# Optimization experiments

Measured on AMD Instinct MI355X. Metric: run time of the kernel, lower is better.

The kernel has to match this reference:

```python
import jax, jax.numpy as jnp
import numpy as np

D = 1024; H = 8; HD = D // H; N_RHS = 4; B = 2; SQ = 1024; SKV = 512
VOCAB = 32000; NL = 6; FF = 4 * D
EPS = 1e-6


def rms(x, w):
    return x * jax.lax.rsqrt(jnp.mean(x * x, axis=-1, keepdims=True) + EPS) * w


def rotate_half(x):
    x1, x2 = jnp.split(x, 2, axis=-1)
    return jnp.concatenate([-x2, x1], axis=-1)


def rope_cos_sin(S):
    inv = 1.0 / (10000.0 ** (jnp.arange(0, HD, 2, dtype=jnp.float32) / HD))
    f = jnp.outer(jnp.arange(S, dtype=jnp.float32), inv)
    f = jnp.concatenate([f, f], axis=-1)  # [S, HD]
    return jnp.cos(f), jnp.sin(f)


def split_heads(t):
    b, s, _ = t.shape
    return t.reshape(b, s, H, HD).swapaxes(1, 2)  # [B,H,S,HD]


def mha_cross(x, kv, in_w, in_b, out_w, out_b):
    # torch nn.MultiheadAttention, batch_first, averaged attn weights
    q = split_heads(x @ in_w[:D].T + in_b[:D])
    k = split_heads(kv @ in_w[D:2 * D].T + in_b[D:2 * D])
    v = split_heads(kv @ in_w[2 * D:].T + in_b[2 * D:])
    a = jax.nn.softmax(jnp.einsum('bhqd,bhkd->bhqk', q, k) / jnp.sqrt(jnp.float32(HD)), axis=-1)
    o = jnp.einsum('bhqk,bhkd->bhqd', a, v).swapaxes(1, 2).reshape(x.shape)
    return o @ out_w.T + out_b, a.mean(axis=1)


def self_attn(x, wq, wk, wv, wo, cos, sin):
    q = split_heads(x @ wq.T)
    k = split_heads(x @ wk.T)
    v = split_heads(x @ wv.T)
    q = q * cos + rotate_half(q) * sin
    k = k * cos + rotate_half(k) * sin
    a = jax.nn.softmax(jnp.einsum('bhqd,bhkd->bhqk', q, k) / jnp.sqrt(jnp.float32(HD)), axis=-1)
    o = jnp.einsum('bhqk,bhkd->bhqd', a, v).swapaxes(1, 2).reshape(x.shape)
    return o @ wo.T


def forward(rh_hiddens, rh_confidences, query_hidden,
            ca_in_w, ca_in_b, ca_out_w, ca_out_b, cross_norm_w,
            ag_w1, ag_b1, ag_w2, ag_b2, ag_norm_w,
            gen_n1, gen_wq, gen_wk, gen_wv, gen_wo, gen_n2, gen_wg, gen_wu, gen_wd,
            gen_norm_w, lm_head_w, m_w1, m_b1, m_w2, m_b2):
    b = query_hidden.shape[0]
    # confidence-weighted KV: rh_hiddens [N,B,S,D], rh_confidences [B,N]
    weighted = rh_hiddens * rh_confidences.T[:, :, None, None]
    all_kv = weighted.transpose(1, 0, 2, 3).reshape(b, N_RHS * SKV, D)

    x = query_hidden
    attn_weights = None
    for i in range(2):
        residual = x
        x = rms(x, cross_norm_w[i])
        x, attn_weights = mha_cross(x, all_kv, ca_in_w[i], ca_in_b[i], ca_out_w[i], ca_out_b[i])
        x = x + residual

    # agreement signal from unweighted per-response summaries
    summaries = rh_hiddens.mean(axis=2).transpose(1, 0, 2).reshape(b, N_RHS * D)
    h = jax.nn.gelu(summaries @ ag_w1.T + ag_b1, approximate=False)
    agreement = rms(h @ ag_w2.T + ag_b2, ag_norm_w)
    x = x + agreement[:, None, :]

    cos, sin = rope_cos_sin(x.shape[1])  # broadcast over [B,H,S,HD]
    for l in range(NL):
        h = rms(x, gen_n1[l])
        x = x + self_attn(h, gen_wq[l], gen_wk[l], gen_wv[l], gen_wo[l], cos, sin)
        h = rms(x, gen_n2[l])
        ff = (jax.nn.silu(h @ gen_wg[l].T) * (h @ gen_wu[l].T)) @ gen_wd[l].T
        x = x + ff

    x = rms(x, gen_norm_w)
    logits = x @ lm_head_w.T
    pooled = x.mean(axis=1)
    meta = jax.nn.gelu(pooled @ m_w1.T + m_b1, approximate=False) @ m_w2.T + m_b2
    return logits, meta, attn_weights


def setup_inputs() -> dict:
    key = jax.random.key(0)
    ks = iter(jax.random.split(key, 40))
    s = 0.02
    rn = lambda *shape: jax.random.normal(next(ks), shape, dtype=jnp.float32) * s
    inp = {
        'rh_hiddens': jax.random.normal(next(ks), (N_RHS, B, SKV, D), dtype=jnp.float32),
        'rh_confidences': jax.random.uniform(next(ks), (B, N_RHS), dtype=jnp.float32),
        'rh_roles': jax.random.randint(next(ks), (B, N_RHS), 0, 8),
        'query_hidden': jax.random.normal(next(ks), (B, SQ, D), dtype=jnp.float32),
        'ca_in_w': rn(2, 3 * D, D), 'ca_in_b': rn(2, 3 * D),
        'ca_out_w': rn(2, D, D), 'ca_out_b': rn(2, D),
        'cross_norm_w': jnp.ones((2, D), jnp.float32),
        'ag_w1': rn(2 * D, N_RHS * D), 'ag_b1': rn(2 * D),
        'ag_w2': rn(D, 2 * D), 'ag_b2': rn(D),
        'ag_norm_w': jnp.ones((D,), jnp.float32),
        'gen_n1': jnp.ones((NL, D), jnp.float32),
        'gen_wq': rn(NL, D, D), 'gen_wk': rn(NL, D, D),
        'gen_wv': rn(NL, D, D), 'gen_wo': rn(NL, D, D),
        'gen_n2': jnp.ones((NL, D), jnp.float32),
        'gen_wg': rn(NL, FF, D), 'gen_wu': rn(NL, FF, D), 'gen_wd': rn(NL, D, FF),
        'gen_norm_w': jnp.ones((D,), jnp.float32),
        'lm_head_w': rn(VOCAB, D),
        'm_w1': rn(D // 4, D), 'm_b1': rn(D // 4),
        'm_w2': rn(3, D // 4), 'm_b2': rn(3),
    }
    return inp


def reference(rh_hiddens, rh_confidences, rh_roles, query_hidden,
              ca_in_w, ca_in_b, ca_out_w, ca_out_b, cross_norm_w,
              ag_w1, ag_b1, ag_w2, ag_b2, ag_norm_w,
              gen_n1, gen_wq, gen_wk, gen_wv, gen_wo, gen_n2, gen_wg, gen_wu, gen_wd,
              gen_norm_w, lm_head_w, m_w1, m_b1, m_w2, m_b2):
    # rh_roles is accepted but unused, matching the torch forward
    return forward(rh_hiddens, rh_confidences, query_hidden,
                   ca_in_w, ca_in_b, ca_out_w, ca_out_b, cross_norm_w,
                   ag_w1, ag_b1, ag_w2, ag_b2, ag_norm_w,
                   gen_n1, gen_wq, gen_wk, gen_wv, gen_wo, gen_n2, gen_wg, gen_wu, gen_wd,
                   gen_norm_w, lm_head_w, m_w1, m_b1, m_w2, m_b2)
```

## Files before the change

### kernel.cpp

```cpp
#include <hip/hip_runtime.h>
#include <math.h>

#define D_     1024
#define H_     8
#define HD_    128
#define NR_    4
#define B_     2
#define SQ_    1024
#define SKV_   512
#define SKVT_  2048
#define VOCAB_ 32000
#define NL_    6
#define FF_    4096
#define EPS_   1e-6f

typedef unsigned short u16;
typedef __attribute__((ext_vector_type(8))) __bf16 bf16x8;
typedef __attribute__((ext_vector_type(4))) float f32x4;

__device__ __forceinline__ u16 f2bf_rn(float f) {
    unsigned u = __float_as_uint(f);
    unsigned r = (u + 0x7FFFu + ((u >> 16) & 1u)) >> 16;
    return (u16)r;
}
__device__ __forceinline__ float bf2f(u16 h) {
    return __uint_as_float(((unsigned)h) << 16);
}
__device__ __forceinline__ void splitf(float v, u16& h, u16& l) {
    h = f2bf_rn(v);
    l = f2bf_rn(v - bf2f(h));
}

__device__ __forceinline__ void glds16(const u16* g, const u16* l) {
    __builtin_amdgcn_global_load_lds(
        (const __attribute__((address_space(1))) void*)g,
        (__attribute__((address_space(3))) void*)l,
        16, 0, 0);
}

enum { CM_F32 = 0, CM_PAIR = 1, CM_PAIRT = 2 };

template<int CMODE>
__global__ __launch_bounds__(256, 2)
void k_gemm_bf(const u16* __restrict__ Ah, const u16* __restrict__ Al,
               int lda, long long sAb, long long sAh,
               const u16* __restrict__ Bh, const u16* __restrict__ Bl,
               int ldb, long long sBb, long long sBh,
               float* __restrict__ Cf, u16* __restrict__ Ch, u16* __restrict__ Cl,
               int ldc, long long sCb, long long sCh,
               int K, int ZH, float scale, const float* __restrict__ bias)
{
    __shared__ u16 lds[16384];

    const int z  = blockIdx.z;
    const int zb = z / ZH, zh = z - zb * ZH;
    const long long offA = zb * sAb + zh * sAh;
    const long long offB = zb * sBb + zh * sBh;
    const long long offC = zb * sCb + zh * sCh;

    const int m0 = blockIdx.y << 7, n0 = blockIdx.x << 7;
    const int tid = threadIdx.x, lane = tid & 63, w = tid >> 6;
    const int wr = w >> 1, wc = w & 1;

    const u16* pAh = Ah + offA; const u16* pAl = Al + offA;
    const u16* pBh = Bh + offB; const u16* pBl = Bl + offB;

    f32x4 acc[4][4];
#pragma unroll
    for (int i = 0; i < 4; ++i)
#pragma unroll
        for (int j = 0; j < 4; ++j) acc[i][j] = (f32x4){0.f, 0.f, 0.f, 0.f};

    const int ks = lane >> 4, lr16 = lane & 15;

    for (int k0 = 0; k0 < K; k0 += 32) {
#pragma unroll
        for (int c = 0; c < 2; ++c) {
            const int chunk = w * 2 + c;
            const int slab = chunk >> 1, hf = chunk & 1;
            const int row = hf * 64 + lane;
            const int lbase = (slab * 128 + hf * 64) * 8;
            const long long ga = (long long)(m0 + row) * lda + (k0 + slab * 8);
            const long long gb = (long long)(n0 + row) * ldb + (k0 + slab * 8);
            glds16(pAh + ga, &lds[lbase]);
            glds16(pAl + ga, &lds[4096 + lbase]);
            glds16(pBh + gb, &lds[8192 + lbase]);
            glds16(pBl + gb, &lds[12288 + lbase]);
        }
        __syncthreads();

        bf16x8 bh[4], bl[4];
#pragma unroll
        for (int nj = 0; nj < 4; ++nj) {
            const int off = (ks * 128 + wc * 64 + nj * 16 + lr16) * 8;
            bh[nj] = *(const bf16x8*)&lds[8192 + off];
            bl[nj] = *(const bf16x8*)&lds[12288 + off];
        }
#pragma unroll
        for (int mi = 0; mi < 4; ++mi) {
            const int off = (ks * 128 + wr * 64 + mi * 16 + lr16) * 8;
            bf16x8 ah = *(const bf16x8*)&lds[off];
            bf16x8 al = *(const bf16x8*)&lds[4096 + off];
#pragma unroll
            for (int nj = 0; nj < 4; ++nj) {
                acc[mi][nj] = __builtin_amdgcn_mfma_f32_16x16x32_bf16(ah, bh[nj], acc[mi][nj], 0, 0, 0);
                acc[mi][nj] = __builtin_amdgcn_mfma_f32_16x16x32_bf16(al, bh[nj], acc[mi][nj], 0, 0, 0);
                acc[mi][nj] = __builtin_amdgcn_mfma_f32_16x16x32_bf16(ah, bl[nj], acc[mi][nj], 0, 0, 0);
            }
        }
        __syncthreads();
    }

#pragma unroll
    for (int mi = 0; mi < 4; ++mi) {
#pragma unroll
        for (int nj = 0; nj < 4; ++nj) {
#pragma unroll
            for (int j = 0; j < 4; ++j) {
                const int row = m0 + wr * 64 + mi * 16 + (lane >> 4) * 4 + j;
                const int col = n0 + wc * 64 + nj * 16 + lr16;
                float v = acc[mi][nj][j] * scale;
                if (bias) v += bias[col];
                if (CMODE == CM_F32) {
                    Cf[offC + (long long)row * ldc + col] = v;
                } else {
                    u16 h, l;
                    splitf(v, h, l);
                    const long long idx = (CMODE == CM_PAIR)
                        ? offC + (long long)row * ldc + col
                        : offC + (long long)col * ldc + row;
                    Ch[idx] = h; Cl[idx] = l;
                }
            }
        }
    }
}

template<bool BTRANS>
__global__ __launch_bounds__(256)
void k_gemm(const float* __restrict__ A, int lda, long long sA,
            const float* __restrict__ B, int ldb, long long sB,
            float* __restrict__ C, int ldc, long long sC,
            int M, int N, int K, float scale, const float* __restrict__ bias)
{
    __shared__ float As[16][128];
    __shared__ float Bs[16][128];

    const int z = blockIdx.z;
    A += (long long)z * sA;
    B += (long long)z * sB;
    C += (long long)z * sC;

    const int m0 = blockIdx.y * 128;
    const int n0 = blockIdx.x * 128;
    const int tid = threadIdx.x;
    const int tm = tid >> 4;
    const int tn = tid & 15;
    const int lr = tid >> 2;
    const int lc = (tid & 3) << 2;

    float acc[8][8];
#pragma unroll
    for (int i = 0; i < 8; ++i)
#pragma unroll
        for (int j = 0; j < 8; ++j) acc[i][j] = 0.f;

    for (int k0 = 0; k0 < K; k0 += 16) {
#pragma unroll
        for (int r = 0; r < 2; ++r) {
            int m = lr + r * 64;
            float4 av = make_float4(0.f, 0.f, 0.f, 0.f);
            if (m0 + m < M)
                av = *(const float4*)(A + (long long)(m0 + m) * lda + (k0 + lc));
            As[lc + 0][m] = av.x; As[lc + 1][m] = av.y;
            As[lc + 2][m] = av.z; As[lc + 3][m] = av.w;
        }
        if (!BTRANS) {
#pragma unroll
            for (int r = 0; r < 2; ++r) {
                int n = lr + r * 64;
                float4 bv = make_float4(0.f, 0.f, 0.f, 0.f);
                if (n0 + n < N)
                    bv = *(const float4*)(B + (long long)(n0 + n) * ldb + (k0 + lc));
                Bs[lc + 0][n] = bv.x; Bs[lc + 1][n] = bv.y;
                Bs[lc + 2][n] = bv.z; Bs[lc + 3][n] = bv.w;
            }
        } else {
            int kk = tid >> 5;
            int nn = (tid & 31) << 2;
#pragma unroll
            for (int r = 0; r < 2; ++r) {
                int k = kk + r * 8;
                float4 bv = make_float4(0.f, 0.f, 0.f, 0.f);
                if (n0 + nn < N)
                    bv = *(const float4*)(B + (long long)(k0 + k) * ldb + (n0 + nn));
                *(float4*)&Bs[k][nn] = bv;
            }
        }
        __syncthreads();

#pragma unroll
        for (int kk = 0; kk < 16; ++kk) {
            float a[8], b[8];
            *(float4*)&a[0] = *(const float4*)&As[kk][tm * 8];
            *(float4*)&a[4] = *(const float4*)&As[kk][tm * 8 + 4];
            *(float4*)&b[0] = *(const float4*)&Bs[kk][tn * 8];
            *(float4*)&b[4] = *(const float4*)&Bs[kk][tn * 8 + 4];
#pragma unroll
            for (int i = 0; i < 8; ++i)
#pragma unroll
                for (int j = 0; j < 8; ++j)
                    acc[i][j] = fmaf(a[i], b[j], acc[i][j]);
        }
        __syncthreads();
    }

#pragma unroll
    for (int i = 0; i < 8; ++i) {
        int m = m0 + tm * 8 + i;
        if (m < M) {
#pragma unroll
            for (int j = 0; j < 8; ++j) {
                int n = n0 + tn * 8 + j;
                if (n < N) {
                    float v = acc[i][j] * scale;
                    if (bias) v += bias[n];
                    C[(long long)m * ldc + n] = v;
                }
            }
        }
    }
}

__global__ __launch_bounds__(256)
void k_rmsnorm(const float* __restrict__ x, const float* __restrict__ w,
               float* __restrict__ yf, u16* __restrict__ yh, u16* __restrict__ yl)
{
    long long row = blockIdx.x;
    const float* xr = x + row * D_;
    int tid = threadIdx.x;

    float4 v = *(const float4*)(xr + tid * 4);
    float ss = v.x * v.x + v.y * v.y + v.z * v.z + v.w * v.w;
#pragma unroll
    for (int off = 32; off >= 1; off >>= 1) ss += __shfl_xor(ss, off);
    __shared__ float red[4];
    if ((tid & 63) == 0) red[tid >> 6] = ss;
    __syncthreads();
    float tot = red[0] + red[1] + red[2] + red[3];
    float sc = 1.0f / sqrtf(tot * (1.0f / D_) + EPS_);

    float4 wv = *(const float4*)(w + tid * 4);
    float o[4];
    o[0] = v.x * sc * wv.x; o[1] = v.y * sc * wv.y;
    o[2] = v.z * sc * wv.z; o[3] = v.w * sc * wv.w;
    if (yf) *(float4*)(yf + row * D_ + tid * 4) = make_float4(o[0], o[1], o[2], o[3]);
    if (yh) {
        u16 h[4], l[4];
#pragma unroll
        for (int i = 0; i < 4; ++i) splitf(o[i], h[i], l[i]);
        uint2 ph = make_uint2((unsigned)h[0] | ((unsigned)h[1] << 16),
                              (unsigned)h[2] | ((unsigned)h[3] << 16));
        uint2 pl = make_uint2((unsigned)l[0] | ((unsigned)l[1] << 16),
                              (unsigned)l[2] | ((unsigned)l[3] << 16));
        ((uint2*)(yh + row * D_))[tid] = ph;
        ((uint2*)(yl + row * D_))[tid] = pl;
    }
}

__global__ __launch_bounds__(256)
void k_softmax(float* __restrict__ S, u16* __restrict__ Ph, u16* __restrict__ Pl,
               int N, int wf32)
{
    __shared__ float buf[2048];
    __shared__ float red[4];
    long long row = blockIdx.x;
    float* p = S + row * (long long)N;
    int tid = threadIdx.x;

    float mx = -1e30f;
    for (int i = tid; i < N; i += 256) { float v = p[i]; buf[i] = v; mx = fmaxf(mx, v); }
#pragma unroll
    for (int off = 32; off >= 1; off >>= 1) mx = fmaxf(mx, __shfl_xor(mx, off));
    if ((tid & 63) == 0) red[tid >> 6] = mx;
    __syncthreads();
    mx = fmaxf(fmaxf(red[0], red[1]), fmaxf(red[2], red[3]));

    float sum = 0.f;
    for (int i = tid; i < N; i += 256) { float e = __expf(buf[i] - mx); buf[i] = e; sum += e; }
#pragma unroll
    for (int off = 32; off >= 1; off >>= 1) sum += __shfl_xor(sum, off);
    __syncthreads();
    if ((tid & 63) == 0) red[tid >> 6] = sum;
    __syncthreads();
    sum = red[0] + red[1] + red[2] + red[3];
    float inv = 1.0f / sum;
    for (int i = tid; i < N; i += 256) {
        float pv = buf[i] * inv;
        if (wf32) p[i] = pv;
        if (Ph) {
            u16 h, l;
            splitf(pv, h, l);
            Ph[row * (long long)N + i] = h;
            Pl[row * (long long)N + i] = l;
        }
    }
}

__global__ void k_weighted_kv(const float* __restrict__ rh,
                              const float* __restrict__ conf,
                              float* __restrict__ kvf,
                              u16* __restrict__ kvh, u16* __restrict__ kvl)
{
    int i4 = blockIdx.x * 256 + threadIdx.x;
    int d4 = i4 & 255;
    int s  = (i4 >> 8) & (SKV_ - 1);
    int n  = (i4 >> 17) & (NR_ - 1);
    int b  = i4 >> 19;
    float c = conf[b * NR_ + n];
    float4 v = ((const float4*)(rh + (((long long)(n * B_ + b) * SKV_ + s) * D_)))[d4];
    v.x *= c; v.y *= c; v.z *= c; v.w *= c;
    if (kvf) ((float4*)kvf)[i4] = v;
    if (kvh) {
        u16 h[4], l[4];
        splitf(v.x, h[0], l[0]); splitf(v.y, h[1], l[1]);
        splitf(v.z, h[2], l[2]); splitf(v.w, h[3], l[3]);
        ((uint2*)kvh)[i4] = make_uint2((unsigned)h[0] | ((unsigned)h[1] << 16),
                                       (unsigned)h[2] | ((unsigned)h[3] << 16));
        ((uint2*)kvl)[i4] = make_uint2((unsigned)l[0] | ((unsigned)l[1] << 16),
                                       (unsigned)l[2] | ((unsigned)l[3] << 16));
    }
}

__global__ void k_summaries(const float* __restrict__ rh, float* __restrict__ sm)
{
    int idx = blockIdx.x * 256 + threadIdx.x;
    int d = idx & (D_ - 1);
    int n = (idx >> 10) & (NR_ - 1);
    int b = idx >> 12;
    const float* p = rh + ((long long)(n * B_ + b) * SKV_) * D_ + d;
    float s = 0.f;
    for (int t = 0; t < SKV_; ++t) s += p[(long long)t * D_];
    sm[idx] = s * (1.0f / SKV_);
}

__global__ void k_attn_mean(const float* __restrict__ S, float* __restrict__ O)
{
    int idx = blockIdx.x * 256 + threadIdx.x;
    float s = 0.f;
#pragma unroll
    for (int h = 0; h < H_; ++h) s += S[(long long)h * SQ_ * SKVT_ + idx];
    O[idx] = s * (1.0f / H_);
}

__global__ void k_rope(float* __restrict__ q, float* __restrict__ k,
                       u16* __restrict__ qh, u16* __restrict__ ql,
                       u16* __restrict__ kh, u16* __restrict__ kl)
{
    int idx = blockIdx.x * 256 + threadIdx.x;
    int j = idx & 63;
    int h = (idx >> 6) & (H_ - 1);
    int s = (idx >> 9) & (SQ_ - 1);
    int b = idx >> 19;
    float inv = __expf(-9.210340371976184f * (float)j * (1.0f / 64.0f));
    float ang = (float)s * inv;
    float sn, cs;
    __sincosf(ang, &sn, &cs);
    long long base = ((long long)(b * SQ_ + s)) * D_ + h * HD_ + j;
    float q1 = q[base], q2 = q[base + 64];
    float qo1 = q1 * cs - q2 * sn;
    float qo2 = q2 * cs + q1 * sn;
    float k1 = k[base], k2 = k[base + 64];
    float ko1 = k1 * cs - k2 * sn;
    float ko2 = k2 * cs + k1 * sn;
    if (qh) {
        u16 h0, l0;
        splitf(qo1, h0, l0); qh[base] = h0;      ql[base] = l0;
        splitf(qo2, h0, l0); qh[base + 64] = h0; ql[base + 64] = l0;
        splitf(ko1, h0, l0); kh[base] = h0;      kl[base] = l0;
        splitf(ko2, h0, l0); kh[base + 64] = h0; kl[base + 64] = l0;
    } else {
        q[base] = qo1; q[base + 64] = qo2;
        k[base] = ko1; k[base + 64] = ko2;
    }
}

__global__ void k_add(float* __restrict__ y, const float* __restrict__ a)
{
    int i = blockIdx.x * 256 + threadIdx.x;
    float4 v = *(const float4*)(y + i * 4);
    float4 u = *(const float4*)(a + i * 4);
    v.x += u.x; v.y += u.y; v.z += u.z; v.w += u.w;
    *(float4*)(y + i * 4) = v;
}

__global__ void k_add_bcast(float* __restrict__ x, const float* __restrict__ ag)
{
    int idx = blockIdx.x * 256 + threadIdx.x;
    int d = idx & (D_ - 1);
    int b = idx >> 20;
    x[idx] += ag[b * D_ + d];
}

__global__ void k_gelu(float* __restrict__ v, int n)
{
    int i = blockIdx.x * 256 + threadIdx.x;
    if (i < n) {
        float x = v[i];
        v[i] = 0.5f * x * (1.0f + erff(x * 0.7071067811865476f));
    }
}

__global__ void k_silu_mul(float* __restrict__ g, const float* __restrict__ u,
                           u16* __restrict__ fh, u16* __restrict__ fl)
{
    int i = blockIdx.x * 256 + threadIdx.x;
    float x = g[i];
    float r = (x / (1.0f + __expf(-x))) * u[i];
    if (fh) {
        u16 h, l;
        splitf(r, h, l);
        fh[i] = h; fl[i] = l;
    } else {
        g[i] = r;
    }
}

__global__ void k_meanpool(const float* __restrict__ h, float* __restrict__ p)
{
    int idx = blockIdx.x * 256 + threadIdx.x;
    int d = idx & (D_ - 1);
    int b = idx >> 10;
    const float* r = h + ((long long)b * SQ_) * D_ + d;
    float s = 0.f;
    for (int t = 0; t < SQ_; ++t) s += r[(long long)t * D_];
    p[idx] = s * (1.0f / SQ_);
}

__global__ void k_split(const float* __restrict__ x, u16* __restrict__ h,
                        u16* __restrict__ l, int n4)
{
    int i = blockIdx.x * 256 + threadIdx.x;
    if (i < n4) {
        float4 v = ((const float4*)x)[i];
        u16 hh[4], ll[4];
        splitf(v.x, hh[0], ll[0]); splitf(v.y, hh[1], ll[1]);
        splitf(v.z, hh[2], ll[2]); splitf(v.w, hh[3], ll[3]);
        ((uint2*)h)[i] = make_uint2((unsigned)hh[0] | ((unsigned)hh[1] << 16),
                                    (unsigned)hh[2] | ((unsigned)hh[3] << 16));
        ((uint2*)l)[i] = make_uint2((unsigned)ll[0] | ((unsigned)ll[1] << 16),
                                    (unsigned)ll[2] | ((unsigned)ll[3] << 16));
    }
}

static void gemm(hipStream_t st,
                 const float* A, int lda, long long sA,
                 const float* B, int ldb, long long sB,
                 float* C, int ldc, long long sC,
                 int Z, int M, int N, int K, float scale, const float* bias,
                 bool btrans)
{
    dim3 g((N + 127) / 128, (M + 127) / 128, Z);
    if (btrans)
        k_gemm<true><<<g, 256, 0, st>>>(A, lda, sA, B, ldb, sB, C, ldc, sC, M, N, K, scale, bias);
    else
        k_gemm<false><<<g, 256, 0, st>>>(A, lda, sA, B, ldb, sB, C, ldc, sC, M, N, K, scale, bias);
}

struct BfMat { const u16* h; const u16* l; int ld; long long sb, sh; };

static void gemm_bf(hipStream_t st, int cmode,
                    BfMat A, BfMat B,
                    float* Cf, u16* Ch, u16* Cl, int ldc, long long sCb, long long sCh,
                    int M, int N, int K, int Z, int ZH, float scale, const float* bias)
{
    dim3 g(N / 128, M / 128, Z);
    if (cmode == CM_F32)
        k_gemm_bf<CM_F32><<<g, 256, 0, st>>>(A.h, A.l, A.ld, A.sb, A.sh,
                                             B.h, B.l, B.ld, B.sb, B.sh,
                                             Cf, Ch, Cl, ldc, sCb, sCh, K, ZH, scale, bias);
    else if (cmode == CM_PAIR)
        k_gemm_bf<CM_PAIR><<<g, 256, 0, st>>>(A.h, A.l, A.ld, A.sb, A.sh,
                                              B.h, B.l, B.ld, B.sb, B.sh,
                                              Cf, Ch, Cl, ldc, sCb, sCh, K, ZH, scale, bias);
    else
        k_gemm_bf<CM_PAIRT><<<g, 256, 0, st>>>(A.h, A.l, A.ld, A.sb, A.sh,
                                               B.h, B.l, B.ld, B.sb, B.sh,
                                               Cf, Ch, Cl, ldc, sCb, sCh, K, ZH, scale, bias);
}

static void split_w(hipStream_t st, const float* w, u16* h, u16* l, long long n)
{
    int n4 = (int)(n >> 2);
    k_split<<<(n4 + 255) / 256, 256, 0, st>>>(w, h, l, n4);
}

extern "C" void kernel_launch(void* const* d_in, const int* in_sizes, int n_in,
                              void* d_out, int out_size, void* d_ws, size_t ws_size,
                              hipStream_t stream)
{
    const float* rh     = (const float*)d_in[0];
    const float* conf   = (const float*)d_in[1];
    const float* qh     = (const float*)d_in[3];
    const float* cainw  = (const float*)d_in[4];
    const float* cainb  = (const float*)d_in[5];
    const float* caoutw = (const float*)d_in[6];
    const float* caoutb = (const float*)d_in[7];
    const float* cnorm  = (const float*)d_in[8];
    const float* agw1   = (const float*)d_in[9];
    const float* agb1   = (const float*)d_in[10];
    const float* agw2   = (const float*)d_in[11];
    const float* agb2   = (const float*)d_in[12];
    const float* agnw   = (const float*)d_in[13];
    const float* n1w    = (const float*)d_in[14];
    const float* wq     = (const float*)d_in[15];
    const float* wk     = (const float*)d_in[16];
    const float* wv     = (const float*)d_in[17];
    const float* wo     = (const float*)d_in[18];
    const float* n2w    = (const float*)d_in[19];
    const float* wg     = (const float*)d_in[20];
    const float* wu     = (const float*)d_in[21];
    const float* wdn    = (const float*)d_in[22];
    const float* gnw    = (const float*)d_in[23];
    const float* lmw    = (const float*)d_in[24];
    const float* mw1    = (const float*)d_in[25];
    const float* mb1    = (const float*)d_in[26];
    const float* mw2    = (const float*)d_in[27];
    const float* mb2    = (const float*)d_in[28];

    float* out    = (float*)d_out;
    float* logits = out;
    float* meta   = out + 65536000;
    float* attnw  = out + 65536006;

    const float iscale = 0.08838834764831845f;
    const size_t MFMA_WS = 276905984ULL;

    if (ws_size >= MFMA_WS) {
        char* base = (char*)d_ws;
        float* xb    = (float*)(base + 0);
        float* qb    = (float*)(base + 8388608);
        float* kb    = (float*)(base + 16777216);
        float* ob    = (float*)(base + 25165824);
        float* R1    = (float*)(base + 33554432);
        float* sml   = (float*)(base + 100663296);
        u16* akvh = (u16*)(base + 100745216);
        u16* akvl = (u16*)(base + 109133824);
        u16* hbh  = (u16*)(base + 117522432);
        u16* hbl  = (u16*)(base + 121716736);
        u16* qph  = (u16*)(base + 125911040);
        u16* qpl  = (u16*)(base + 130105344);
        u16* kph  = (u16*)(base + 134299648);
        u16* kpl  = (u16*)(base + 142688256);
        u16* vth  = (u16*)(base + 151076864);
        u16* vtl  = (u16*)(base + 159465472);
        u16* ctxh = (u16*)(base + 167854080);
        u16* ctxl = (u16*)(base + 172048384);
        u16* R2h  = (u16*)(base + 176242688);
        u16* R2l  = (u16*)(base + 209797120);
        u16* wsh  = (u16*)(base + 243351552);
        u16* wsl  = (u16*)(base + 260128768);

        float* sb  = R1;
        float* ffg = R1;
        float* ffu = R1 + 8388608;
        u16* ph = R2h; u16* pl = R2l;
        u16* ffh = R2h; u16* ffl = R2h + 16777216 / 2 * 0 + 16777216;
        ffh = R2h; ffl = R2l;

        float* summ   = sml;
        float* agh    = summ + 8192;
        float* ago    = agh + 4096;
        float* agr    = ago + 2048;
        float* pooled = agr + 2048;
        float* mbuf   = pooled + 2048;

        k_weighted_kv<<<4096, 256, 0, stream>>>(rh, conf, nullptr, akvh, akvl);
        k_summaries<<<32, 256, 0, stream>>>(rh, summ);
        hipMemcpyAsync(xb, qh, (size_t)2097152 * 4, hipMemcpyDeviceToDevice, stream);

        BfMat Ahb  = {hbh, hbl, D_, 0, 0};
        BfMat Akv  = {akvh, akvl, D_, 0, 0};
        BfMat Wscr = {wsh, wsl, D_, 0, 0};

        for (int i = 0; i < 2; ++i) {
            const float* inw = cainw + (size_t)i * 3 * D_ * D_;
            const float* inb = cainb + (size_t)i * 3 * D_;
            k_rmsnorm<<<B_ * SQ_, 256, 0, stream>>>(xb, cnorm + i * D_, nullptr, hbh, hbl);
            split_w(stream, inw, wsh, wsl, 1048576);
            gemm_bf(stream, CM_PAIR, Ahb, Wscr, nullptr, qph, qpl, D_, 0, 0,
                    B_ * SQ_, D_, D_, 1, 1, 1.f, inb);
            split_w(stream, inw + 1048576, wsh, wsl, 1048576);
            gemm_bf(stream, CM_PAIR, Akv, Wscr, nullptr, kph, kpl, D_, 0, 0,
                    B_ * SKVT_, D_, D_, 1, 1, 1.f, inb + D_);
            split_w(stream, inw + 2097152, wsh, wsl, 1048576);
            gemm_bf(stream, CM_PAIRT, Akv, Wscr, nullptr, vth, vtl, B_ * SKVT_, 0, 0,
                    B_ * SKVT_, D_, D_, 1, 1, 1.f, inb + 2 * D_);

            for (int b = 0; b < B_; ++b) {
                BfMat Aq = {qph + (size_t)b * SQ_ * D_, qpl + (size_t)b * SQ_ * D_, D_, 0, HD_};
                BfMat Bk = {kph + (size_t)b * SKVT_ * D_, kpl + (size_t)b * SKVT_ * D_, D_, 0, HD_};
                gemm_bf(stream, CM_F32, Aq, Bk, sb, nullptr, nullptr,
                        SKVT_, 0, (long long)SQ_ * SKVT_,
                        SQ_, SKVT_, HD_, H_, H_, iscale, nullptr);
                k_softmax<<<H_ * SQ_, 256, 0, stream>>>(sb, ph, pl, SKVT_, (i == 1) ? 1 : 0);
                if (i == 1)
                    k_attn_mean<<<8192, 256, 0, stream>>>(sb, attnw + (size_t)b * SQ_ * SKVT_);
                BfMat Ap = {ph, pl, SKVT_, 0, (long long)SQ_ * SKVT_};
                BfMat Bv = {vth + (size_t)b * SKVT_, vtl + (size_t)b * SKVT_,
                            B_ * SKVT_, 0, (long long)HD_ * B_ * SKVT_};
                gemm_bf(stream, CM_PAIR, Ap, Bv, nullptr,
                        ctxh + (size_t)b * SQ_ * D_, ctxl + (size_t)b * SQ_ * D_,
                        D_, 0, HD_, SQ_, HD_, SKVT_, H_, H_, 1.f, nullptr);
            }
            split_w(stream, caoutw + (size_t)i * D_ * D_, wsh, wsl, 1048576);
            BfMat Actx = {ctxh, ctxl, D_, 0, 0};
            gemm_bf(stream, CM_F32, Actx, Wscr, ob, nullptr, nullptr, D_, 0, 0,
                    B_ * SQ_, D_, D_, 1, 1, 1.f, caoutb + i * D_);
            k_add<<<2048, 256, 0, stream>>>(xb, ob);
        }

        gemm(stream, summ, NR_ * D_, 0, agw1, NR_ * D_, 0, agh, 2 * D_, 0,
             1, B_, 2 * D_, NR_ * D_, 1.f, agb1, false);
        k_gelu<<<16, 256, 0, stream>>>(agh, B_ * 2 * D_);
        gemm(stream, agh, 2 * D_, 0, agw2, 2 * D_, 0, ago, D_, 0,
             1, B_, D_, 2 * D_, 1.f, agb2, false);
        k_rmsnorm<<<B_, 256, 0, stream>>>(ago, agnw, agr, nullptr, nullptr);
        k_add_bcast<<<8192, 256, 0, stream>>>(xb, agr);

        for (int l = 0; l < NL_; ++l) {
            const size_t woff = (size_t)l * D_ * D_;
            const size_t foff = (size_t)l * FF_ * D_;
            k_rmsnorm<<<B_ * SQ_, 256, 0, stream>>>(xb, n1w + l * D_, nullptr, hbh, hbl);
            split_w(stream, wq + woff, wsh, wsl, 1048576);
            gemm_bf(stream, CM_F32, Ahb, Wscr, qb, nullptr, nullptr, D_, 0, 0,
                    B_ * SQ_, D_, D_, 1, 1, 1.f, nullptr);
            split_w(stream, wk + woff, wsh, wsl, 1048576);
            gemm_bf(stream, CM_F32, Ahb, Wscr, kb, nullptr, nullptr, D_, 0, 0,
                    B_ * SQ_, D_, D_, 1, 1, 1.f, nullptr);
            split_w(stream, wv + woff, wsh, wsl, 1048576);
            gemm_bf(stream, CM_PAIRT, Ahb, Wscr, nullptr, vth, vtl, B_ * SQ_, 0, 0,
                    B_ * SQ_, D_, D_, 1, 1, 1.f, nullptr);
            k_rope<<<4096, 256, 0, stream>>>(qb, kb, qph, qpl, kph, kpl);

            {
                BfMat Aq = {qph, qpl, D_, (long long)SQ_ * D_, HD_};
                BfMat Bk = {kph, kpl, D_, (long long)SQ_ * D_, HD_};
                gemm_bf(stream, CM_F32, Aq, Bk, sb, nullptr, nullptr,
                        SQ_, (long long)H_ * SQ_ * SQ_, (long long)SQ_ * SQ_,
                        SQ_, SQ_, HD_, B_ * H_, H_, iscale, nullptr);
            }
            k_softmax<<<B_ * H_ * SQ_, 256, 0, stream>>>(sb, ph, pl, SQ_, 0);
            {
                BfMat Ap = {ph, pl, SQ_, (long long)H_ * SQ_ * SQ_, (long long)SQ_ * SQ_};
                BfMat Bv = {vth, vtl, B_ * SQ_, SQ_, (long long)HD_ * B_ * SQ_};
                gemm_bf(stream, CM_PAIR, Ap, Bv, nullptr, ctxh, ctxl,
                        D_, (long long)SQ_ * D_, HD_,
                        SQ_, HD_, SQ_, B_ * H_, H_, 1.f, nullptr);
            }
            split_w(stream, wo + woff, wsh, wsl, 1048576);
            {
                BfMat Actx = {ctxh, ctxl, D_, 0, 0};
                gemm_bf(stream, CM_F32, Actx, Wscr, ob, nullptr, nullptr, D_, 0, 0,
                        B_ * SQ_, D_, D_, 1, 1, 1.f, nullptr);
            }
            k_add<<<2048, 256, 0, stream>>>(xb, ob);

            k_rmsnorm<<<B_ * SQ_, 256, 0, stream>>>(xb, n2w + l * D_, nullptr, hbh, hbl);
            split_w(stream, wg + foff, wsh, wsl, 4194304);
            gemm_bf(stream, CM_F32, Ahb, Wscr, ffg, nullptr, nullptr, FF_, 0, 0,
                    B_ * SQ_, FF_, D_, 1, 1, 1.f, nullptr);
            split_w(stream, wu + foff, wsh, wsl, 4194304);
            gemm_bf(stream, CM_F32, Ahb, Wscr, ffu, nullptr, nullptr, FF_, 0, 0,
                    B_ * SQ_, FF_, D_, 1, 1, 1.f, nullptr);
            k_silu_mul<<<32768, 256, 0, stream>>>(ffg, ffu, ffh, ffl);
            split_w(stream, wdn + foff, wsh, wsl, 4194304);
            {
                BfMat Aff = {ffh, ffl, FF_, 0, 0};
                BfMat Wd  = {wsh, wsl, FF_, 0, 0};
                gemm_bf(stream, CM_F32, Aff, Wd, ob, nullptr, nullptr, D_, 0, 0,
                        B_ * SQ_, D_, FF_, 1, 1, 1.f, nullptr);
            }
            k_add<<<2048, 256, 0, stream>>>(xb, ob);
        }

        k_rmsnorm<<<B_ * SQ_, 256, 0, stream>>>(xb, gnw, qb, hbh, hbl);
        {
            int chunks[4] = {8192, 8192, 8192, 7424};
            int coff = 0;
            for (int c = 0; c < 4; ++c) {
                split_w(stream, lmw + (size_t)coff * D_, wsh, wsl, (long long)chunks[c] * D_);
                gemm_bf(stream, CM_F32, Ahb, Wscr, logits + coff, nullptr, nullptr,
                        VOCAB_, 0, 0, B_ * SQ_, chunks[c], D_, 1, 1, 1.f, nullptr);
                coff += chunks[c];
            }
        }
        k_meanpool<<<8, 256, 0, stream>>>(qb, pooled);
        gemm(stream, pooled, D_, 0, mw1, D_, 0, mbuf, 256, 0,
             1, B_, 256, D_, 1.f, mb1, false);
        k_gelu<<<2, 256, 0, stream>>>(mbuf, B_ * 256);
        gemm(stream, mbuf, 256, 0, mw2, 256, 0, meta, 3, 0,
             1, B_, 3, 256, 1.f, mb2, false);
        return;
    }

    float* ws    = (float*)d_ws;
    float* allkv = ws;
    float* xb    = allkv + 4194304;
    float* hb    = xb + 2097152;
    float* qb    = hb + 2097152;
    float* ctx   = qb + 2097152;
    float* ob    = ctx + 2097152;
    float* kb    = ob + 2097152;
    float* vb    = kb + 4194304;
    float* sb    = vb + 4194304;
    float* ffg   = sb;
    float* ffu   = sb + 8388608;
    float* sml2  = sb + 16777216;
    float* summ  = sml2;
    float* agh   = summ + 8192;
    float* ago   = agh + 4096;
    float* agr   = ago + 2048;
    float* pooled= agr + 2048;
    float* mbuf  = pooled + 2048;
    if (ws_size < (size_t)39911424 * 4) return;

    k_weighted_kv<<<4096, 256, 0, stream>>>(rh, conf, allkv, nullptr, nullptr);
    k_summaries<<<32, 256, 0, stream>>>(rh, summ);
    hipMemcpyAsync(xb, qh, (size_t)2097152 * 4, hipMemcpyDeviceToDevice, stream);

    for (int i = 0; i < 2; ++i) {
        const float* inw = cainw + (size_t)i * 3 * D_ * D_;
        const float* inb = cainb + (size_t)i * 3 * D_;
        k_rmsnorm<<<B_ * SQ_, 256, 0, stream>>>(xb, cnorm + i * D_, hb, nullptr, nullptr);
        gemm(stream, hb, D_, 0, inw, D_, 0, qb, D_, 0, 1, B_ * SQ_, D_, D_, 1.f, inb, false);
        gemm(stream, allkv, D_, 0, inw + 1048576, D_, 0, kb, D_, 0, 1, B_ * SKVT_, D_, D_, 1.f, inb + D_, false);
        gemm(stream, allkv, D_, 0, inw + 2097152, D_, 0, vb, D_, 0, 1, B_ * SKVT_, D_, D_, 1.f, inb + 2 * D_, false);
        for (int b = 0; b < B_; ++b) {
            gemm(stream, qb + (size_t)b * SQ_ * D_, D_, HD_,
                 kb + (size_t)b * SKVT_ * D_, D_, HD_,
                 sb, SKVT_, (long long)SQ_ * SKVT_,
                 H_, SQ_, SKVT_, HD_, iscale, nullptr, false);
            k_softmax<<<H_ * SQ_, 256, 0, stream>>>(sb, nullptr, nullptr, SKVT_, 1);
            if (i == 1)
                k_attn_mean<<<8192, 256, 0, stream>>>(sb, attnw + (size_t)b * SQ_ * SKVT_);
            gemm(stream, sb, SKVT_, (long long)SQ_ * SKVT_,
                 vb + (size_t)b * SKVT_ * D_, D_, HD_,
                 ctx + (size_t)b * SQ_ * D_, D_, HD_,
                 H_, SQ_, HD_, SKVT_, 1.f, nullptr, true);
        }
        gemm(stream, ctx, D_, 0, caoutw + (size_t)i * D_ * D_, D_, 0, ob, D_, 0,
             1, B_ * SQ_, D_, D_, 1.f, caoutb + i * D_, false);
        k_add<<<2048, 256, 0, stream>>>(xb, ob);
    }

    gemm(stream, summ, NR_ * D_, 0, agw1, NR_ * D_, 0, agh, 2 * D_, 0,
         1, B_, 2 * D_, NR_ * D_, 1.f, agb1, false);
    k_gelu<<<16, 256, 0, stream>>>(agh, B_ * 2 * D_);
    gemm(stream, agh, 2 * D_, 0, agw2, 2 * D_, 0, ago, D_, 0,
         1, B_, D_, 2 * D_, 1.f, agb2, false);
    k_rmsnorm<<<B_, 256, 0, stream>>>(ago, agnw, agr, nullptr, nullptr);
    k_add_bcast<<<8192, 256, 0, stream>>>(xb, agr);

    for (int l = 0; l < NL_; ++l) {
        const size_t woff = (size_t)l * D_ * D_;
        const size_t foff = (size_t)l * FF_ * D_;
        k_rmsnorm<<<B_ * SQ_, 256, 0, stream>>>(xb, n1w + l * D_, hb, nullptr, nullptr);
        gemm(stream, hb, D_, 0, wq + woff, D_, 0, qb, D_, 0, 1, B_ * SQ_, D_, D_, 1.f, nullptr, false);
        gemm(stream, hb, D_, 0, wk + woff, D_, 0, kb, D_, 0, 1, B_ * SQ_, D_, D_, 1.f, nullptr, false);
        gemm(stream, hb, D_, 0, wv + woff, D_, 0, vb, D_, 0, 1, B_ * SQ_, D_, D_, 1.f, nullptr, false);
        k_rope<<<4096, 256, 0, stream>>>(qb, kb, nullptr, nullptr, nullptr, nullptr);
        for (int b = 0; b < B_; ++b) {
            gemm(stream, qb + (size_t)b * SQ_ * D_, D_, HD_,
                 kb + (size_t)b * SQ_ * D_, D_, HD_,
                 sb, SQ_, (long long)SQ_ * SQ_,
                 H_, SQ_, SQ_, HD_, iscale, nullptr, false);
            k_softmax<<<H_ * SQ_, 256, 0, stream>>>(sb, nullptr, nullptr, SQ_, 1);
            gemm(stream, sb, SQ_, (long long)SQ_ * SQ_,
                 vb + (size_t)b * SQ_ * D_, D_, HD_,
                 ctx + (size_t)b * SQ_ * D_, D_, HD_,
                 H_, SQ_, HD_, SQ_, 1.f, nullptr, true);
        }
        gemm(stream, ctx, D_, 0, wo + woff, D_, 0, ob, D_, 0, 1, B_ * SQ_, D_, D_, 1.f, nullptr, false);
        k_add<<<2048, 256, 0, stream>>>(xb, ob);

        k_rmsnorm<<<B_ * SQ_, 256, 0, stream>>>(xb, n2w + l * D_, hb, nullptr, nullptr);
        gemm(stream, hb, D_, 0, wg + foff, D_, 0, ffg, FF_, 0, 1, B_ * SQ_, FF_, D_, 1.f, nullptr, false);
        gemm(stream, hb, D_, 0, wu + foff, D_, 0, ffu, FF_, 0, 1, B_ * SQ_, FF_, D_, 1.f, nullptr, false);
        k_silu_mul<<<32768, 256, 0, stream>>>(ffg, ffu, nullptr, nullptr);
        gemm(stream, ffg, FF_, 0, wdn + foff, FF_, 0, ob, D_, 0, 1, B_ * SQ_, D_, FF_, 1.f, nullptr, false);
        k_add<<<2048, 256, 0, stream>>>(xb, ob);
    }

    k_rmsnorm<<<B_ * SQ_, 256, 0, stream>>>(xb, gnw, hb, nullptr, nullptr);
    gemm(stream, hb, D_, 0, lmw, D_, 0, logits, VOCAB_, 0,
         1, B_ * SQ_, VOCAB_, D_, 1.f, nullptr, false);
    k_meanpool<<<8, 256, 0, stream>>>(hb, pooled);
    gemm(stream, pooled, D_, 0, mw1, D_, 0, mbuf, 256, 0,
         1, B_, 256, D_, 1.f, mb1, false);
    k_gelu<<<2, 256, 0, stream>>>(mbuf, B_ * 256);
    gemm(stream, mbuf, 256, 0, mw2, 256, 0, meta, 3, 0,
         1, B_, 3, 256, 1.f, mb2, false);
}
```

Before: 8.396 ms.

## Fuse residual adds into GEMM epilogue, add skinny GEMV and parallel meanpool

The residual add is folded into the epilogue of the output-projection GEMMs, which now write into xb in place, so the separate k_add passes disappear. The tiny aggregator and meta-head matmuls with M=2 move from the 128-tile fp32 GEMM to a wave-per-output dot-product kernel that also applies GELU. Meanpool becomes a two-pass parallel reduction instead of 8 blocks doing serial column sums. Launch bounds for the bf16 GEMM rise to 3 blocks per SM, which may add register pressure or spills.

```diff
diff --git a/kernel.cpp b/kernel.cpp
--- a/kernel.cpp
+++ b/kernel.cpp
@@ -41,14 +41,15 @@
 enum { CM_F32 = 0, CM_PAIR = 1, CM_PAIRT = 2 };
 
 template<int CMODE>
-__global__ __launch_bounds__(256, 2)
+__global__ __launch_bounds__(256, 3)
 void k_gemm_bf(const u16* __restrict__ Ah, const u16* __restrict__ Al,
                int lda, long long sAb, long long sAh,
                const u16* __restrict__ Bh, const u16* __restrict__ Bl,
                int ldb, long long sBb, long long sBh,
                float* __restrict__ Cf, u16* __restrict__ Ch, u16* __restrict__ Cl,
                int ldc, long long sCb, long long sCh,
-               int K, int ZH, float scale, const float* __restrict__ bias)
+               int K, int ZH, float scale, const float* __restrict__ bias,
+               const float* __restrict__ resid)
 {
     __shared__ u16 lds[16384];
 
@@ -122,7 +123,9 @@
                 float v = acc[mi][nj][j] * scale;
                 if (bias) v += bias[col];
                 if (CMODE == CM_F32) {
-                    Cf[offC + (long long)row * ldc + col] = v;
+                    const long long idx = offC + (long long)row * ldc + col;
+                    if (resid) v += resid[idx];
+                    Cf[idx] = v;
                 } else {
                     u16 h, l;
                     splitf(v, h, l);
@@ -133,6 +136,34 @@
                 }
             }
         }
+    }
+}
+
+__global__ __launch_bounds__(256)
+void k_skinny(const float* __restrict__ A, int lda,
+              const float* __restrict__ B, int ldb,
+              const float* __restrict__ bias,
+              float* __restrict__ C, int ldc,
+              int M, int N, int K, int gelu)
+{
+    int w = (blockIdx.x * 256 + threadIdx.x) >> 6;
+    int lane = threadIdx.x & 63;
+    if (w >= M * N) return;
+    int m = w / N, n = w - m * N;
+    const float* a = A + (long long)m * lda;
+    const float* b = B + (long long)n * ldb;
+    float s = 0.f;
+    for (int k = lane * 4; k < K; k += 256) {
+        float4 av = *(const float4*)(a + k);
+        float4 bv = *(const float4*)(b + k);
+        s += av.x * bv.x + av.y * bv.y + av.z * bv.z + av.w * bv.w;
+    }
+#pragma unroll
+    for (int off = 32; off >= 1; off >>= 1) s += __shfl_xor(s, off);
+    if (lane == 0) {
+        if (bias) s += bias[n];
+        if (gelu) s = 0.5f * s * (1.0f + erff(s * 0.7071067811865476f));
+        C[(long long)m * ldc + n] = s;
     }
 }
 
@@ -437,6 +468,28 @@
     p[idx] = s * (1.0f / SQ_);
 }
 
+__global__ void k_meanpool_p1(const float* __restrict__ h, float* __restrict__ part)
+{
+    int b = blockIdx.x >> 4, sc = blockIdx.x & 15;
+    int t = threadIdx.x;
+    const float* base = h + ((long long)b * SQ_ + sc * 64) * D_;
+    float4 s = make_float4(0.f, 0.f, 0.f, 0.f);
+    for (int r = 0; r < 64; ++r) {
+        float4 v = ((const float4*)(base + (long long)r * D_))[t];
+        s.x += v.x; s.y += v.y; s.z += v.z; s.w += v.w;
+    }
+    ((float4*)(part + (long long)(b * 16 + sc) * D_))[t] = s;
+}
+__global__ void k_meanpool_p2(const float* __restrict__ part, float* __restrict__ p)
+{
+    int idx = blockIdx.x * 256 + threadIdx.x;
+    int b = idx >> 10, d = idx & 1023;
+    float s = 0.f;
+#pragma unroll
+    for (int c = 0; c < 16; ++c) s += part[(long long)(b * 16 + c) * D_ + d];
+    p[idx] = s * (1.0f / SQ_);
+}
+
 __global__ void k_split(const float* __restrict__ x, u16* __restrict__ h,
                         u16* __restrict__ l, int n4)
 {
@@ -472,27 +525,35 @@
 static void gemm_bf(hipStream_t st, int cmode,
                     BfMat A, BfMat B,
                     float* Cf, u16* Ch, u16* Cl, int ldc, long long sCb, long long sCh,
-                    int M, int N, int K, int Z, int ZH, float scale, const float* bias)
+                    int M, int N, int K, int Z, int ZH, float scale, const float* bias,
+                    const float* resid)
 {
     dim3 g(N / 128, M / 128, Z);
     if (cmode == CM_F32)
         k_gemm_bf<CM_F32><<<g, 256, 0, st>>>(A.h, A.l, A.ld, A.sb, A.sh,
                                              B.h, B.l, B.ld, B.sb, B.sh,
-                                             Cf, Ch, Cl, ldc, sCb, sCh, K, ZH, scale, bias);
+                                             Cf, Ch, Cl, ldc, sCb, sCh, K, ZH, scale, bias, resid);
     else if (cmode == CM_PAIR)
         k_gemm_bf<CM_PAIR><<<g, 256, 0, st>>>(A.h, A.l, A.ld, A.sb, A.sh,
                                               B.h, B.l, B.ld, B.sb, B.sh,
-                                              Cf, Ch, Cl, ldc, sCb, sCh, K, ZH, scale, bias);
+                                              Cf, Ch, Cl, ldc, sCb, sCh, K, ZH, scale, bias, nullptr);
     else
         k_gemm_bf<CM_PAIRT><<<g, 256, 0, st>>>(A.h, A.l, A.ld, A.sb, A.sh,
                                                B.h, B.l, B.ld, B.sb, B.sh,
-                                               Cf, Ch, Cl, ldc, sCb, sCh, K, ZH, scale, bias);
+                                               Cf, Ch, Cl, ldc, sCb, sCh, K, ZH, scale, bias, nullptr);
 }
 
 static void split_w(hipStream_t st, const float* w, u16* h, u16* l, long long n)
 {
     int n4 = (int)(n >> 2);
     k_split<<<(n4 + 255) / 256, 256, 0, st>>>(w, h, l, n4);
+}
+
+static void skinny(hipStream_t st, const float* A, int lda, const float* B, int ldb,
+                   const float* bias, float* C, int ldc, int M, int N, int K, int gelu)
+{
+    int blocks = (M * N * 64 + 255) / 256;
+    k_skinny<<<blocks, 256, 0, st>>>(A, lda, B, ldb, bias, C, ldc, M, N, K, gelu);
 }
 
 extern "C" void kernel_launch(void* const* d_in, const int* in_sizes, int n_in,
@@ -565,8 +626,7 @@
         float* ffg = R1;
         float* ffu = R1 + 8388608;
         u16* ph = R2h; u16* pl = R2l;
-        u16* ffh = R2h; u16* ffl = R2h + 16777216 / 2 * 0 + 16777216;
-        ffh = R2h; ffl = R2l;
+        u16* ffh = R2h; u16* ffl = R2l;
 
         float* summ   = sml;
         float* agh    = summ + 8192;
@@ -574,6 +634,7 @@
         float* agr    = ago + 2048;
         float* pooled = agr + 2048;
         float* mbuf   = pooled + 2048;
+        float* mpart  = ob;
 
         k_weighted_kv<<<4096, 256, 0, stream>>>(rh, conf, nullptr, akvh, akvl);
         k_summaries<<<32, 256, 0, stream>>>(rh, summ);
@@ -589,20 +650,20 @@
             k_rmsnorm<<<B_ * SQ_, 256, 0, stream>>>(xb, cnorm + i * D_, nullptr, hbh, hbl);
             split_w(stream, inw, wsh, wsl, 1048576);
             gemm_bf(stream, CM_PAIR, Ahb, Wscr, nullptr, qph, qpl, D_, 0, 0,
-                    B_ * SQ_, D_, D_, 1, 1, 1.f, inb);
+                    B_ * SQ_, D_, D_, 1, 1, 1.f, inb, nullptr);
             split_w(stream, inw + 1048576, wsh, wsl, 1048576);
             gemm_bf(stream, CM_PAIR, Akv, Wscr, nullptr, kph, kpl, D_, 0, 0,
-                    B_ * SKVT_, D_, D_, 1, 1, 1.f, inb + D_);
+                    B_ * SKVT_, D_, D_, 1, 1, 1.f, inb + D_, nullptr);
             split_w(stream, inw + 2097152, wsh, wsl, 1048576);
             gemm_bf(stream, CM_PAIRT, Akv, Wscr, nullptr, vth, vtl, B_ * SKVT_, 0, 0,
-                    B_ * SKVT_, D_, D_, 1, 1, 1.f, inb + 2 * D_);
+                    B_ * SKVT_, D_, D_, 1, 1, 1.f, inb + 2 * D_, nullptr);
 
             for (int b = 0; b < B_; ++b) {
                 BfMat Aq = {qph + (size_t)b * SQ_ * D_, qpl + (size_t)b * SQ_ * D_, D_, 0, HD_};
                 BfMat Bk = {kph + (size_t)b * SKVT_ * D_, kpl + (size_t)b * SKVT_ * D_, D_, 0, HD_};
                 gemm_bf(stream, CM_F32, Aq, Bk, sb, nullptr, nullptr,
                         SKVT_, 0, (long long)SQ_ * SKVT_,
-                        SQ_, SKVT_, HD_, H_, H_, iscale, nullptr);
+                        SQ_, SKVT_, HD_, H_, H_, iscale, nullptr, nullptr);
                 k_softmax<<<H_ * SQ_, 256, 0, stream>>>(sb, ph, pl, SKVT_, (i == 1) ? 1 : 0);
                 if (i == 1)
                     k_attn_mean<<<8192, 256, 0, stream>>>(sb, attnw + (size_t)b * SQ_ * SKVT_);
@@ -611,20 +672,18 @@
                             B_ * SKVT_, 0, (long long)HD_ * B_ * SKVT_};
                 gemm_bf(stream, CM_PAIR, Ap, Bv, nullptr,
                         ctxh + (size_t)b * SQ_ * D_, ctxl + (size_t)b * SQ_ * D_,
-                        D_, 0, HD_, SQ_, HD_, SKVT_, H_, H_, 1.f, nullptr);
+                        D_, 0, HD_, SQ_, HD_, SKVT_, H_, H_, 1.f, nullptr, nullptr);
             }
             split_w(stream, caoutw + (size_t)i * D_ * D_, wsh, wsl, 1048576);
             BfMat Actx = {ctxh, ctxl, D_, 0, 0};
-            gemm_bf(stream, CM_F32, Actx, Wscr, ob, nullptr, nullptr, D_, 0, 0,
-                    B_ * SQ_, D_, D_, 1, 1, 1.f, caoutb + i * D_);
-            k_add<<<2048, 256, 0, stream>>>(xb, ob);
-        }
-
-        gemm(stream, summ, NR_ * D_, 0, agw1, NR_ * D_, 0, agh, 2 * D_, 0,
-             1, B_, 2 * D_, NR_ * D_, 1.f, agb1, false);
-        k_gelu<<<16, 256, 0, stream>>>(agh, B_ * 2 * D_);
-        gemm(stream, agh, 2 * D_, 0, agw2, 2 * D_, 0, ago, D_, 0,
-             1, B_, D_, 2 * D_, 1.f, agb2, false);
+            gemm_bf(stream, CM_F32, Actx, Wscr, xb, nullptr, nullptr, D_, 0, 0,
+                    B_ * SQ_, D_, D_, 1, 1, 1.f, caoutb + i * D_, xb);
+        }
+
+        skinny(stream, summ, NR_ * D_, agw1, NR_ * D_, agb1, agh, 2 * D_,
+               B_, 2 * D_, NR_ * D_, 1);
+        skinny(stream, agh, 2 * D_, agw2, 2 * D_, agb2, ago, D_,
+               B_, D_, 2 * D_, 0);
         k_rmsnorm<<<B_, 256, 0, stream>>>(ago, agnw, agr, nullptr, nullptr);
         k_add_bcast<<<8192, 256, 0, stream>>>(xb, agr);
 
@@ -634,13 +693,13 @@
             k_rmsnorm<<<B_ * SQ_, 256, 0, stream>>>(xb, n1w + l * D_, nullptr, hbh, hbl);
             split_w(stream, wq + woff, wsh, wsl, 1048576);
             gemm_bf(stream, CM_F32, Ahb, Wscr, qb, nullptr, nullptr, D_, 0, 0,
-                    B_ * SQ_, D_, D_, 1, 1, 1.f, nullptr);
+                    B_ * SQ_, D_, D_, 1, 1, 1.f, nullptr, nullptr);
             split_w(stream, wk + woff, wsh, wsl, 1048576);
             gemm_bf(stream, CM_F32, Ahb, Wscr, kb, nullptr, nullptr, D_, 0, 0,
-                    B_ * SQ_, D_, D_, 1, 1, 1.f, nullptr);
+                    B_ * SQ_, D_, D_, 1, 1, 1.f, nullptr, nullptr);
             split_w(stream, wv + woff, wsh, wsl, 1048576);
             gemm_bf(stream, CM_PAIRT, Ahb, Wscr, nullptr, vth, vtl, B_ * SQ_, 0, 0,
-                    B_ * SQ_, D_, D_, 1, 1, 1.f, nullptr);
+                    B_ * SQ_, D_, D_, 1, 1, 1.f, nullptr, nullptr);
             k_rope<<<4096, 256, 0, stream>>>(qb, kb, qph, qpl, kph, kpl);
 
             {
@@ -648,7 +707,7 @@
                 BfMat Bk = {kph, kpl, D_, (long long)SQ_ * D_, HD_};
                 gemm_bf(stream, CM_F32, Aq, Bk, sb, nullptr, nullptr,
                         SQ_, (long long)H_ * SQ_ * SQ_, (long long)SQ_ * SQ_,
-                        SQ_, SQ_, HD_, B_ * H_, H_, iscale, nullptr);
+                        SQ_, SQ_, HD_, B_ * H_, H_, iscale, nullptr, nullptr);
             }
             k_softmax<<<B_ * H_ * SQ_, 256, 0, stream>>>(sb, ph, pl, SQ_, 0);
             {
@@ -656,32 +715,30 @@
                 BfMat Bv = {vth, vtl, B_ * SQ_, SQ_, (long long)HD_ * B_ * SQ_};
                 gemm_bf(stream, CM_PAIR, Ap, Bv, nullptr, ctxh, ctxl,
                         D_, (long long)SQ_ * D_, HD_,
-                        SQ_, HD_, SQ_, B_ * H_, H_, 1.f, nullptr);
+                        SQ_, HD_, SQ_, B_ * H_, H_, 1.f, nullptr, nullptr);
             }
             split_w(stream, wo + woff, wsh, wsl, 1048576);
             {
                 BfMat Actx = {ctxh, ctxl, D_, 0, 0};
-                gemm_bf(stream, CM_F32, Actx, Wscr, ob, nullptr, nullptr, D_, 0, 0,
-                        B_ * SQ_, D_, D_, 1, 1, 1.f, nullptr);
-            }
-            k_add<<<2048, 256, 0, stream>>>(xb, ob);
+                gemm_bf(stream, CM_F32, Actx, Wscr, xb, nullptr, nullptr, D_, 0, 0,
+                        B_ * SQ_, D_, D_, 1, 1, 1.f, nullptr, xb);
+            }
 
             k_rmsnorm<<<B_ * SQ_, 256, 0, stream>>>(xb, n2w + l * D_, nullptr, hbh, hbl);
             split_w(stream, wg + foff, wsh, wsl, 4194304);
             gemm_bf(stream, CM_F32, Ahb, Wscr, ffg, nullptr, nullptr, FF_, 0, 0,
-                    B_ * SQ_, FF_, D_, 1, 1, 1.f, nullptr);
+                    B_ * SQ_, FF_, D_, 1, 1, 1.f, nullptr, nullptr);
             split_w(stream, wu + foff, wsh, wsl, 4194304);
             gemm_bf(stream, CM_F32, Ahb, Wscr, ffu, nullptr, nullptr, FF_, 0, 0,
-                    B_ * SQ_, FF_, D_, 1, 1, 1.f, nullptr);
+                    B_ * SQ_, FF_, D_, 1, 1, 1.f, nullptr, nullptr);
             k_silu_mul<<<32768, 256, 0, stream>>>(ffg, ffu, ffh, ffl);
             split_w(stream, wdn + foff, wsh, wsl, 4194304);
             {
                 BfMat Aff = {ffh, ffl, FF_, 0, 0};
                 BfMat Wd  = {wsh, wsl, FF_, 0, 0};
-                gemm_bf(stream, CM_F32, Aff, Wd, ob, nullptr, nullptr, D_, 0, 0,
-                        B_ * SQ_, D_, FF_, 1, 1, 1.f, nullptr);
-            }
-            k_add<<<2048, 256, 0, stream>>>(xb, ob);
+                gemm_bf(stream, CM_F32, Aff, Wd, xb, nullptr, nullptr, D_, 0, 0,
+                        B_ * SQ_, D_, FF_, 1, 1, 1.f, nullptr, xb);
+            }
         }
 
         k_rmsnorm<<<B_ * SQ_, 256, 0, stream>>>(xb, gnw, qb, hbh, hbl);
@@ -691,16 +748,14 @@
             for (int c = 0; c < 4; ++c) {
                 split_w(stream, lmw + (size_t)coff * D_, wsh, wsl, (long long)chunks[c] * D_);
                 gemm_bf(stream, CM_F32, Ahb, Wscr, logits + coff, nullptr, nullptr,
-                        VOCAB_, 0, 0, B_ * SQ_, chunks[c], D_, 1, 1, 1.f, nullptr);
+                        VOCAB_, 0, 0, B_ * SQ_, chunks[c], D_, 1, 1, 1.f, nullptr, nullptr);
                 coff += chunks[c];
             }
         }
-        k_meanpool<<<8, 256, 0, stream>>>(qb, pooled);
-        gemm(stream, pooled, D_, 0, mw1, D_, 0, mbuf, 256, 0,
-             1, B_, 256, D_, 1.f, mb1, false);
-        k_gelu<<<2, 256, 0, stream>>>(mbuf, B_ * 256);
-        gemm(stream, mbuf, 256, 0, mw2, 256, 0, meta, 3, 0,
-             1, B_, 3, 256, 1.f, mb2, false);
+        k_meanpool_p1<<<32, 256, 0, stream>>>(qb, mpart);
+        k_meanpool_p2<<<8, 256, 0, stream>>>(mpart, pooled);
+        skinny(stream, pooled, D_, mw1, D_, mb1, mbuf, 256, B_, 256, D_, 1);
+        skinny(stream, mbuf, 256, mw2, 256, mb2, meta, 3, B_, 3, 256, 0);
         return;
     }
 
```

New measurement: 7.400 ms. 1.13x faster.
